# Kernel tuning notes

Measured on AMD Instinct MI355X. Metric: run time of the kernel, lower is better.

Reference implementation:

```python
import jax, jax.numpy as jnp
import numpy as np

D_IN = 1024
D_OUT = 1024
CTX_LEN = 2048
BATCH = 4
SEQ = 2048


def setup_inputs() -> dict:
    key = jax.random.key(0)
    kx, kq, kk, kv = jax.random.split(key, 4)
    x = jax.random.normal(kx, (BATCH, SEQ, D_IN), dtype=jnp.float32)
    s = 1.0 / np.sqrt(D_IN)
    # torch nn.Linear weight is (d_out, d_in); store transposed for x @ W
    W_q = jax.random.uniform(kq, (D_IN, D_OUT), dtype=jnp.float32, minval=-s, maxval=s)
    W_k = jax.random.uniform(kk, (D_IN, D_OUT), dtype=jnp.float32, minval=-s, maxval=s)
    W_v = jax.random.uniform(kv, (D_IN, D_OUT), dtype=jnp.float32, minval=-s, maxval=s)
    return {"x": x, "W_q": W_q, "W_k": W_k, "W_v": W_v}


def reference(x, W_q, W_k, W_v):
    b, n, _ = x.shape
    d_out = W_q.shape[1]
    q = x @ W_q            # [b, n, d_out]
    k = x @ W_k
    v = x @ W_v
    scores = jnp.einsum('bqd,bkd->bqk', q, k)  # [b, n, n]
    causal = jnp.triu(jnp.ones((n, n), dtype=bool), k=1)
    scores = jnp.where(causal, -jnp.inf, scores)
    attn = jax.nn.softmax(scores / jnp.sqrt(jnp.float32(d_out)), axis=-1)
    # dropout p=0.0 -> identity
    return jnp.einsum('bqk,bkd->bqd', attn, v)
```

## Files before the change

### kernel.cpp

```cpp
#include <hip/hip_runtime.h>
#include <hip/hip_bf16.h>

#define BATCH 4
#define SEQ   2048
#define DIN   1024
#define DOUT  1024
#define N3    3072
#define MTOT  (BATCH*SEQ)

typedef __hip_bfloat16 bf16;
typedef __attribute__((ext_vector_type(8))) short bf16x8;
typedef __attribute__((ext_vector_type(4))) float f32x4;

#define MFMA(a,b,c) __builtin_amdgcn_mfma_f32_16x16x32_bf16(a,b,c,0,0,0)

union pack4 { bf16 h[4]; uint2 u2; };
union pack8 { bf16 h[8]; bf16x8 v; };

__device__ __forceinline__ void gl16(const bf16* g, bf16* l)
{
    __builtin_amdgcn_global_load_lds(
        (const __attribute__((address_space(1))) void*)g,
        (__attribute__((address_space(3))) void*)l, 16, 0, 0);
}


__global__ __launch_bounds__(256)
void k_prep(const float* __restrict__ x, const float* __restrict__ Wq,
            const float* __restrict__ Wk, const float* __restrict__ Wv,
            bf16* __restrict__ xb, bf16* __restrict__ Wt,
            float* __restrict__ RS)
{
    __shared__ bf16 t[64][68];
    const int bid = blockIdx.x;
    if (bid < 8192) {
        long i = ((long)bid * 256 + threadIdx.x) * 4;
        float4 v = *(const float4*)(x + i);
        pack4 o;
        o.h[0] = __float2bfloat16(v.x);
        o.h[1] = __float2bfloat16(v.y);
        o.h[2] = __float2bfloat16(v.z);
        o.h[3] = __float2bfloat16(v.w);
        *(uint2*)(xb + i) = o.u2;
        return;
    }
    if (bid >= 8960) {
        int i = (bid - 8960) * 1024 + threadIdx.x * 4;
        *(float4*)(RS + i) = make_float4(0.f, 0.f, 0.f, 0.f);
        return;
    }
    const int idx = bid - 8192;
    const int mat = idx >> 8;
    const int rem = idx & 255;
    const int k0 = (rem >> 4) * 64, n0 = (rem & 15) * 64;
    const float* W = (mat == 0) ? Wq : ((mat == 1) ? Wk : Wv);
#pragma unroll
    for (int p = 0; p < 4; ++p) {
        int kr = p * 16 + (threadIdx.x >> 4);
        int c4 = (threadIdx.x & 15) * 4;
        float4 v = *(const float4*)&W[(long)(k0 + kr) * DOUT + n0 + c4];
        t[c4 + 0][kr] = __float2bfloat16(v.x);
        t[c4 + 1][kr] = __float2bfloat16(v.y);
        t[c4 + 2][kr] = __float2bfloat16(v.z);
        t[c4 + 3][kr] = __float2bfloat16(v.w);
    }
    __syncthreads();
    bf16* O = Wt + (long)mat * DIN * DOUT;
#pragma unroll
    for (int i = 0; i < 2; ++i) {
        int l = threadIdx.x + i * 256;
        int n = l >> 3, c8 = (l & 7) * 8;
        pack8 o;
#pragma unroll
        for (int j = 0; j < 8; ++j) o.h[j] = t[n][c8 + j];
        *(bf16x8*)&O[(long)(n0 + n) * DIN + k0 + c8] = o.v;
    }
}


template<int DIAG>
__device__ __forceinline__ void gemm_core(
    const bf16* __restrict__ Ab, long lda,
    const bf16* __restrict__ Bb, long ldb,
    int nk, bf16* __restrict__ As, bf16* __restrict__ Bs,
    f32x4 acc[4][4])
{
    const int tid  = threadIdx.x;
    const int lane = tid & 63;
    const int wave = tid >> 6;
    const int wm = (wave >> 1) * 64;
    const int wn = (wave & 1) * 64;
    const int r  = lane & 15;
    const int qd = lane >> 4;

    const bool skipWave = DIAG && (wn > wm);
    const bool sameOff  = DIAG && (wn == wm);

    const int row0 = tid >> 3;
    const int c    = (tid & 7) ^ (row0 & 7);
    const long aoff = (long)row0 * lda + c * 8;
    const long boff = (long)row0 * ldb + c * 8;
    const long astep = 32 * lda, bstep = 32 * ldb;
    bf16* dA = &As[tid * 8];
    bf16* dB = &Bs[tid * 8];

    for (int kk = 0; kk < nk; ++kk) {
        const bf16* A = Ab + kk * 64 + aoff;
        const bf16* B = Bb + kk * 64 + boff;
#pragma unroll
        for (int i = 0; i < 4; ++i) {
            gl16(A + i * astep, dA + i * 2048);
            gl16(B + i * bstep, dB + i * 2048);
        }
        __syncthreads();
        if (!skipWave) {
#pragma unroll
            for (int ks = 0; ks < 2; ++ks) {
                const int slot = ((ks * 4 + qd) ^ (r & 7)) * 8;
                bf16x8 af[4], bv[4];
#pragma unroll
                for (int mi = 0; mi < 4; ++mi)
                    af[mi] = *(const bf16x8*)&As[(wm + mi * 16 + r) * 64 + slot];
#pragma unroll
                for (int ni = 0; ni < 4; ++ni)
                    bv[ni] = *(const bf16x8*)&Bs[(wn + ni * 16 + r) * 64 + slot];
#pragma unroll
                for (int mi = 0; mi < 4; ++mi)
#pragma unroll
                    for (int ni = 0; ni < 4; ++ni) {
                        if (sameOff && ni > mi) continue;
                        acc[mi][ni] = MFMA(af[mi], bv[ni], acc[mi][ni]);
                    }
            }
        }
        __syncthreads();
    }
}


__global__ __launch_bounds__(256)
void k_gemm_qkv(const bf16* __restrict__ xb, const bf16* __restrict__ Wt,
                bf16* __restrict__ QK, bf16* __restrict__ Vt)
{
    __shared__ __align__(16) bf16 smem[17408];
    bf16* As = smem;
    bf16* Bs = smem + 8192;
    const int m0 = blockIdx.y * 128, n0 = blockIdx.x * 128;
    f32x4 acc[4][4] = {};
    gemm_core<0>(xb + (long)m0 * DIN, DIN, Wt + (long)n0 * DIN, DIN, DIN / 64, As, Bs, acc);

    const int tid = threadIdx.x;
    const int lane = tid & 63, wave = tid >> 6;
    const int wm = (wave >> 1) * 64, wn = (wave & 1) * 64;
    const int r = lane & 15, qd = lane >> 4;

    if (n0 < 2048) {
#pragma unroll
        for (int mi = 0; mi < 4; ++mi)
#pragma unroll
            for (int ni = 0; ni < 4; ++ni)
#pragma unroll
                for (int j = 0; j < 4; ++j) {
                    int row = m0 + wm + mi * 16 + qd * 4 + j;
                    int col = n0 + wn + ni * 16 + r;
                    QK[(long)row * 2048 + col] = __float2bfloat16(acc[mi][ni][j]);
                }
    } else {
        const int ld = 136;
        bf16* T = smem;
#pragma unroll
        for (int mi = 0; mi < 4; ++mi)
#pragma unroll
            for (int ni = 0; ni < 4; ++ni) {
                pack4 p;
#pragma unroll
                for (int j = 0; j < 4; ++j) p.h[j] = __float2bfloat16(acc[mi][ni][j]);
                int d_l = wn + ni * 16 + r;
                int s_l = wm + mi * 16 + qd * 4;
                *(uint2*)&T[d_l * ld + s_l] = p.u2;
            }
        __syncthreads();
        const int n0v = n0 - 2048;
        const int bb = m0 >> 11;
        const int s0 = m0 & 2047;
        bf16* Ob = Vt + (long)bb * DOUT * SEQ + s0;
#pragma unroll
        for (int p = 0; p < 8; ++p) {
            int l = tid + p * 256;
            int d = l >> 4, s8 = (l & 15) * 8;
            bf16x8 vv = *(const bf16x8*)&T[d * ld + s8];
            *(bf16x8*)&Ob[(long)(n0v + d) * SEQ + s8] = vv;
        }
    }
}


__global__ __launch_bounds__(256, 3)
void k_gemm_scores(const bf16* __restrict__ QK, bf16* __restrict__ P,
                   float* __restrict__ rowSum)
{
    const int bid = blockIdx.x;
    int b, qt, kt;
    if (bid < 480) {
        b = bid & 3;
        int u = bid >> 2;
        qt = 15;
        while (u >= qt) { u -= qt; --qt; }
        kt = u;
    } else {
        int i = bid - 480;
        b = i & 3;
        qt = kt = i >> 2;
    }

    __shared__ __align__(16) bf16 smem[17408];
    bf16* As = smem;
    bf16* Bs = smem + 8192;
    const bf16* A  = QK + (long)b * SEQ * 2048;
    const bf16* Bt = A + 1024;
    f32x4 acc[4][4] = {};
    if (bid < 480)
        gemm_core<0>(A + (long)qt * 128 * 2048, 2048, Bt + (long)kt * 128 * 2048,
                     2048, DIN / 64, As, Bs, acc);
    else
        gemm_core<1>(A + (long)qt * 128 * 2048, 2048, Bt + (long)kt * 128 * 2048,
                     2048, DIN / 64, As, Bs, acc);

    bf16* Pb = P + (long)b * SEQ * SEQ;
    float* RS = rowSum + b * SEQ;
    const int tid = threadIdx.x;
    const int lane = tid & 63, wave = tid >> 6;
    const int wm = (wave >> 1) * 64, wn = (wave & 1) * 64;
    const int r = lane & 15, qd = lane >> 4;

    const int ld = 136;
    bf16* T = smem;

    float rp[4][4];
#pragma unroll
    for (int mi = 0; mi < 4; ++mi)
#pragma unroll
        for (int j = 0; j < 4; ++j) rp[mi][j] = 0.f;

#pragma unroll
    for (int mi = 0; mi < 4; ++mi)
#pragma unroll
        for (int ni = 0; ni < 4; ++ni)
#pragma unroll
            for (int j = 0; j < 4; ++j) {
                int row_l = wm + mi * 16 + qd * 4 + j;
                int col_l = wn + ni * 16 + r;
                int row = qt * 128 + row_l;
                int col = kt * 128 + col_l;
                float e = (col > row) ? 0.f : __expf(acc[mi][ni][j] * 0.03125f);
                rp[mi][j] += e;
                T[row_l * ld + col_l] = __float2bfloat16(e);
            }
#pragma unroll
    for (int d = 1; d < 16; d <<= 1)
#pragma unroll
        for (int mi = 0; mi < 4; ++mi)
#pragma unroll
            for (int j = 0; j < 4; ++j)
                rp[mi][j] += __shfl_xor(rp[mi][j], d, 64);
    if (r == 0) {
#pragma unroll
        for (int mi = 0; mi < 4; ++mi)
#pragma unroll
            for (int j = 0; j < 4; ++j) {
                int row = qt * 128 + wm + mi * 16 + qd * 4 + j;
                atomicAdd(&RS[row], rp[mi][j]);
            }
    }
    __syncthreads();
#pragma unroll
    for (int p = 0; p < 8; ++p) {
        int l = tid + p * 256;
        int row_l = l >> 4, c8 = (l & 15) * 8;
        bf16x8 vv = *(const bf16x8*)&T[row_l * ld + c8];
        *(bf16x8*)&Pb[(long)(qt * 128 + row_l) * SEQ + kt * 128 + c8] = vv;
    }
}


__global__ __launch_bounds__(256, 3)
void k_gemm_pv(const bf16* __restrict__ P, const bf16* __restrict__ Vt,
               const float* __restrict__ rowSum, float* __restrict__ O)
{
    const int bid = blockIdx.x;
    const int h   = bid & 255;
    const int qt  = (bid < 256) ? (15 - (h >> 5)) : (h >> 5);
    const int b   = (h >> 3) & 3;
    const int nt  = h & 7;
    __shared__ __align__(16) bf16 As[128 * 64];
    __shared__ __align__(16) bf16 Bs[128 * 64];
    const bf16* A  = P + (long)b * SEQ * SEQ + (long)qt * 128 * SEQ;
    const bf16* Bt = Vt + (long)b * DOUT * SEQ;
    const int nk = (qt + 1) * 2;
    f32x4 acc[4][4] = {};
    gemm_core<0>(A, SEQ, Bt + (long)nt * 128 * SEQ, SEQ, nk, As, Bs, acc);

    float* Ob = O + (long)b * SEQ * DOUT;
    const float* RS = rowSum + b * SEQ;
    const int lane = threadIdx.x & 63, wave = threadIdx.x >> 6;
    const int wm = (wave >> 1) * 64, wn = (wave & 1) * 64;
    const int r = lane & 15, qd = lane >> 4;
#pragma unroll
    for (int mi = 0; mi < 4; ++mi)
#pragma unroll
        for (int j = 0; j < 4; ++j) {
            int row = qt * 128 + wm + mi * 16 + qd * 4 + j;
            float inv = 1.0f / RS[row];
#pragma unroll
            for (int ni = 0; ni < 4; ++ni) {
                int col = nt * 128 + wn + ni * 16 + r;
                Ob[(long)row * DOUT + col] = acc[mi][ni][j] * inv;
            }
        }
}


extern "C" void kernel_launch(void* const* d_in, const int* in_sizes, int n_in,
                              void* d_out, int out_size, void* d_ws, size_t ws_size,
                              hipStream_t stream)
{
    const float* x  = (const float*)d_in[0];
    const float* Wq = (const float*)d_in[1];
    const float* Wk = (const float*)d_in[2];
    const float* Wv = (const float*)d_in[3];
    float* out = (float*)d_out;

    char* ws = (char*)d_ws;
    bf16*  xb = (bf16*)(ws);
    bf16*  Wt = (bf16*)(ws + 16777216);
    bf16*  QK = (bf16*)(ws + 23068672);
    bf16*  Vt = (bf16*)(ws + 56623104);
    bf16*  P  = (bf16*)(ws + 73400320);
    float* RS = (float*)(ws + 106954752);

    k_prep<<<dim3(8192 + 768 + 8), 256, 0, stream>>>(x, Wq, Wk, Wv, xb, Wt, RS);
    k_gemm_qkv<<<dim3(N3 / 128, MTOT / 128), 256, 0, stream>>>(xb, Wt, QK, Vt);
    k_gemm_scores<<<dim3(544), 256, 0, stream>>>(QK, P, RS);
    k_gemm_pv<<<dim3(512), 256, 0, stream>>>(P, Vt, RS, out);
}
```

Baseline: 211.0 us.

## Fold Wq·Wkᵀ into one matrix so scores use x instead of K

Rewrites the score computation using the identity q·kᵀ = x·(Wq·Wkᵀ)·xᵀ. The prep kernel computes M = Wq·Wkᵀ once in bf16, the projection GEMM produces x·M and V, and the scores GEMM reads x directly in place of K. This removes one third of the projection GEMM work and the K buffer, and stages scores reads through a narrower row stride. The cost is a small extra 1024³ GEMM inside prep, and rounding the folded matrix to bf16 changes numerics.

```diff
diff --git a/kernel.cpp b/kernel.cpp
--- a/kernel.cpp
+++ b/kernel.cpp
@@ -5,7 +5,6 @@
 #define SEQ   2048
 #define DIN   1024
 #define DOUT  1024
-#define N3    3072
 #define MTOT  (BATCH*SEQ)
 
 typedef __hip_bfloat16 bf16;
@@ -28,13 +27,77 @@
 __global__ __launch_bounds__(256)
 void k_prep(const float* __restrict__ x, const float* __restrict__ Wq,
             const float* __restrict__ Wk, const float* __restrict__ Wv,
-            bf16* __restrict__ xb, bf16* __restrict__ Wt,
-            float* __restrict__ RS)
-{
-    __shared__ bf16 t[64][68];
+            bf16* __restrict__ xb, bf16* __restrict__ Wtv,
+            bf16* __restrict__ Mt, float* __restrict__ RS)
+{
+    __shared__ __align__(16) bf16 smem[8192];
     const int bid = blockIdx.x;
-    if (bid < 8192) {
-        long i = ((long)bid * 256 + threadIdx.x) * 4;
+    const int tid = threadIdx.x;
+
+    if (bid < 256) {
+        bf16* As = smem;
+        bf16* Bs = smem + 4096;
+        const int m0 = (bid >> 4) * 64;
+        const int n0 = (bid & 15) * 64;
+        const int lane = tid & 63, wave = tid >> 6;
+        const int wm = (wave >> 1) * 32, wn = (wave & 1) * 32;
+        const int r = lane & 15, qd = lane >> 4;
+        f32x4 acc[2][2] = {};
+        for (int kk = 0; kk < 16; ++kk) {
+#pragma unroll
+            for (int j = 0; j < 2; ++j) {
+                int ch = tid * 2 + j;
+                int row = ch >> 3, cc = ch & 7;
+                int dst = row * 64 + ((cc ^ (row & 7)) * 8);
+                const float* pa = Wk + (long)(m0 + row) * 1024 + kk * 64 + cc * 8;
+                float4 a0 = *(const float4*)pa, a1 = *(const float4*)(pa + 4);
+                pack8 o;
+                o.h[0] = __float2bfloat16(a0.x); o.h[1] = __float2bfloat16(a0.y);
+                o.h[2] = __float2bfloat16(a0.z); o.h[3] = __float2bfloat16(a0.w);
+                o.h[4] = __float2bfloat16(a1.x); o.h[5] = __float2bfloat16(a1.y);
+                o.h[6] = __float2bfloat16(a1.z); o.h[7] = __float2bfloat16(a1.w);
+                *(bf16x8*)&As[dst] = o.v;
+                const float* pb = Wq + (long)(n0 + row) * 1024 + kk * 64 + cc * 8;
+                float4 b0 = *(const float4*)pb, b1 = *(const float4*)(pb + 4);
+                o.h[0] = __float2bfloat16(b0.x); o.h[1] = __float2bfloat16(b0.y);
+                o.h[2] = __float2bfloat16(b0.z); o.h[3] = __float2bfloat16(b0.w);
+                o.h[4] = __float2bfloat16(b1.x); o.h[5] = __float2bfloat16(b1.y);
+                o.h[6] = __float2bfloat16(b1.z); o.h[7] = __float2bfloat16(b1.w);
+                *(bf16x8*)&Bs[dst] = o.v;
+            }
+            __syncthreads();
+#pragma unroll
+            for (int ks = 0; ks < 2; ++ks) {
+                const int slot = ((ks * 4 + qd) ^ (r & 7)) * 8;
+                bf16x8 af[2], bv[2];
+#pragma unroll
+                for (int mi = 0; mi < 2; ++mi)
+                    af[mi] = *(const bf16x8*)&As[(wm + mi * 16 + r) * 64 + slot];
+#pragma unroll
+                for (int ni = 0; ni < 2; ++ni)
+                    bv[ni] = *(const bf16x8*)&Bs[(wn + ni * 16 + r) * 64 + slot];
+#pragma unroll
+                for (int mi = 0; mi < 2; ++mi)
+#pragma unroll
+                    for (int ni = 0; ni < 2; ++ni)
+                        acc[mi][ni] = MFMA(af[mi], bv[ni], acc[mi][ni]);
+            }
+            __syncthreads();
+        }
+#pragma unroll
+        for (int mi = 0; mi < 2; ++mi)
+#pragma unroll
+            for (int ni = 0; ni < 2; ++ni)
+#pragma unroll
+                for (int j = 0; j < 4; ++j) {
+                    int row = m0 + wm + mi * 16 + qd * 4 + j;
+                    int col = n0 + wn + ni * 16 + r;
+                    Mt[(long)row * 1024 + col] = __float2bfloat16(acc[mi][ni][j]);
+                }
+        return;
+    }
+    if (bid < 8448) {
+        long i = ((long)(bid - 256) * 256 + tid) * 4;
         float4 v = *(const float4*)(x + i);
         pack4 o;
         o.h[0] = __float2bfloat16(v.x);
@@ -44,36 +107,33 @@
         *(uint2*)(xb + i) = o.u2;
         return;
     }
-    if (bid >= 8960) {
-        int i = (bid - 8960) * 1024 + threadIdx.x * 4;
+    if (bid >= 8704) {
+        int i = (bid - 8704) * 1024 + tid * 4;
         *(float4*)(RS + i) = make_float4(0.f, 0.f, 0.f, 0.f);
         return;
     }
-    const int idx = bid - 8192;
-    const int mat = idx >> 8;
-    const int rem = idx & 255;
-    const int k0 = (rem >> 4) * 64, n0 = (rem & 15) * 64;
-    const float* W = (mat == 0) ? Wq : ((mat == 1) ? Wk : Wv);
+    const int idx = bid - 8448;
+    const int k0 = (idx >> 4) * 64, n0 = (idx & 15) * 64;
+    bf16* t = smem;
 #pragma unroll
     for (int p = 0; p < 4; ++p) {
-        int kr = p * 16 + (threadIdx.x >> 4);
-        int c4 = (threadIdx.x & 15) * 4;
-        float4 v = *(const float4*)&W[(long)(k0 + kr) * DOUT + n0 + c4];
-        t[c4 + 0][kr] = __float2bfloat16(v.x);
-        t[c4 + 1][kr] = __float2bfloat16(v.y);
-        t[c4 + 2][kr] = __float2bfloat16(v.z);
-        t[c4 + 3][kr] = __float2bfloat16(v.w);
+        int kr = p * 16 + (tid >> 4);
+        int c4 = (tid & 15) * 4;
+        float4 v = *(const float4*)&Wv[(long)(k0 + kr) * DOUT + n0 + c4];
+        t[(c4 + 0) * 68 + kr] = __float2bfloat16(v.x);
+        t[(c4 + 1) * 68 + kr] = __float2bfloat16(v.y);
+        t[(c4 + 2) * 68 + kr] = __float2bfloat16(v.z);
+        t[(c4 + 3) * 68 + kr] = __float2bfloat16(v.w);
     }
     __syncthreads();
-    bf16* O = Wt + (long)mat * DIN * DOUT;
 #pragma unroll
     for (int i = 0; i < 2; ++i) {
-        int l = threadIdx.x + i * 256;
+        int l = tid + i * 256;
         int n = l >> 3, c8 = (l & 7) * 8;
         pack8 o;
 #pragma unroll
-        for (int j = 0; j < 8; ++j) o.h[j] = t[n][c8 + j];
-        *(bf16x8*)&O[(long)(n0 + n) * DIN + k0 + c8] = o.v;
+        for (int j = 0; j < 8; ++j) o.h[j] = t[n * 68 + c8 + j];
+        *(bf16x8*)&Wtv[(long)(n0 + n) * DIN + k0 + c8] = o.v;
     }
 }
 
@@ -139,22 +199,27 @@
 
 
 __global__ __launch_bounds__(256)
-void k_gemm_qkv(const bf16* __restrict__ xb, const bf16* __restrict__ Wt,
-                bf16* __restrict__ QK, bf16* __restrict__ Vt)
+void k_gemm_qkv(const bf16* __restrict__ xb, const bf16* __restrict__ Mt,
+                const bf16* __restrict__ Wtv, bf16* __restrict__ Qp,
+                bf16* __restrict__ Vt)
 {
     __shared__ __align__(16) bf16 smem[17408];
     bf16* As = smem;
     bf16* Bs = smem + 8192;
-    const int m0 = blockIdx.y * 128, n0 = blockIdx.x * 128;
+    const int m0 = blockIdx.y * 128;
+    const int bx = blockIdx.x;
+    const int n0 = bx * 128;
+    const bf16* Bpan = (bx < 8) ? (Mt + (long)n0 * DIN)
+                                : (Wtv + (long)(n0 - 1024) * DIN);
     f32x4 acc[4][4] = {};
-    gemm_core<0>(xb + (long)m0 * DIN, DIN, Wt + (long)n0 * DIN, DIN, DIN / 64, As, Bs, acc);
+    gemm_core<0>(xb + (long)m0 * DIN, DIN, Bpan, DIN, DIN / 64, As, Bs, acc);
 
     const int tid = threadIdx.x;
     const int lane = tid & 63, wave = tid >> 6;
     const int wm = (wave >> 1) * 64, wn = (wave & 1) * 64;
     const int r = lane & 15, qd = lane >> 4;
 
-    if (n0 < 2048) {
+    if (bx < 8) {
 #pragma unroll
         for (int mi = 0; mi < 4; ++mi)
 #pragma unroll
@@ -163,7 +228,7 @@
                 for (int j = 0; j < 4; ++j) {
                     int row = m0 + wm + mi * 16 + qd * 4 + j;
                     int col = n0 + wn + ni * 16 + r;
-                    QK[(long)row * 2048 + col] = __float2bfloat16(acc[mi][ni][j]);
+                    Qp[(long)row * 1024 + col] = __float2bfloat16(acc[mi][ni][j]);
                 }
     } else {
         const int ld = 136;
@@ -180,7 +245,7 @@
                 *(uint2*)&T[d_l * ld + s_l] = p.u2;
             }
         __syncthreads();
-        const int n0v = n0 - 2048;
+        const int n0v = n0 - 1024;
         const int bb = m0 >> 11;
         const int s0 = m0 & 2047;
         bf16* Ob = Vt + (long)bb * DOUT * SEQ + s0;
@@ -196,35 +261,31 @@
 
 
 __global__ __launch_bounds__(256, 3)
-void k_gemm_scores(const bf16* __restrict__ QK, bf16* __restrict__ P,
-                   float* __restrict__ rowSum)
+void k_gemm_scores(const bf16* __restrict__ Qp, const bf16* __restrict__ xb,
+                   bf16* __restrict__ P, float* __restrict__ rowSum)
 {
     const int bid = blockIdx.x;
-    int b, qt, kt;
-    if (bid < 480) {
-        b = bid & 3;
-        int u = bid >> 2;
+    int b, qt, kt, u = -1, d = -1;
+    if      (bid < 256) u = bid;
+    else if (bid < 288) d = bid - 256;
+    else if (bid < 512) u = bid - 32;
+    else                d = bid - 480;
+    if (u >= 0) {
+        b = u & 3;
+        int v = u >> 2;
         qt = 15;
-        while (u >= qt) { u -= qt; --qt; }
-        kt = u;
-    } else {
-        int i = bid - 480;
-        b = i & 3;
-        qt = kt = i >> 2;
-    }
+        while (v >= qt) { v -= qt; --qt; }
+        kt = v;
+    } else { b = d & 3; qt = kt = d >> 2; }
 
     __shared__ __align__(16) bf16 smem[17408];
     bf16* As = smem;
     bf16* Bs = smem + 8192;
-    const bf16* A  = QK + (long)b * SEQ * 2048;
-    const bf16* Bt = A + 1024;
+    const bf16* A  = Qp + (long)(b * SEQ + qt * 128) * 1024;
+    const bf16* Bt = xb + (long)(b * SEQ + kt * 128) * 1024;
     f32x4 acc[4][4] = {};
-    if (bid < 480)
-        gemm_core<0>(A + (long)qt * 128 * 2048, 2048, Bt + (long)kt * 128 * 2048,
-                     2048, DIN / 64, As, Bs, acc);
-    else
-        gemm_core<1>(A + (long)qt * 128 * 2048, 2048, Bt + (long)kt * 128 * 2048,
-                     2048, DIN / 64, As, Bs, acc);
+    if (u >= 0) gemm_core<0>(A, 1024, Bt, 1024, DIN / 64, As, Bs, acc);
+    else        gemm_core<1>(A, 1024, Bt, 1024, DIN / 64, As, Bs, acc);
 
     bf16* Pb = P + (long)b * SEQ * SEQ;
     float* RS = rowSum + b * SEQ;
@@ -257,12 +318,12 @@
                 T[row_l * ld + col_l] = __float2bfloat16(e);
             }
 #pragma unroll
-    for (int d = 1; d < 16; d <<= 1)
+    for (int dd = 1; dd < 16; dd <<= 1)
 #pragma unroll
         for (int mi = 0; mi < 4; ++mi)
 #pragma unroll
             for (int j = 0; j < 4; ++j)
-                rp[mi][j] += __shfl_xor(rp[mi][j], d, 64);
+                rp[mi][j] += __shfl_xor(rp[mi][j], dd, 64);
     if (r == 0) {
 #pragma unroll
         for (int mi = 0; mi < 4; ++mi)
@@ -331,15 +392,17 @@
     float* out = (float*)d_out;
 
     char* ws = (char*)d_ws;
-    bf16*  xb = (bf16*)(ws);
-    bf16*  Wt = (bf16*)(ws + 16777216);
-    bf16*  QK = (bf16*)(ws + 23068672);
-    bf16*  Vt = (bf16*)(ws + 56623104);
-    bf16*  P  = (bf16*)(ws + 73400320);
-    float* RS = (float*)(ws + 106954752);
-
-    k_prep<<<dim3(8192 + 768 + 8), 256, 0, stream>>>(x, Wq, Wk, Wv, xb, Wt, RS);
-    k_gemm_qkv<<<dim3(N3 / 128, MTOT / 128), 256, 0, stream>>>(xb, Wt, QK, Vt);
-    k_gemm_scores<<<dim3(544), 256, 0, stream>>>(QK, P, RS);
+    bf16*  xb  = (bf16*)(ws);
+    bf16*  Wtv = (bf16*)(ws + 16777216);
+    bf16*  Mt  = (bf16*)(ws + 18874368);
+    bf16*  Qp  = (bf16*)(ws + 20971520);
+    bf16*  Vt  = (bf16*)(ws + 37748736);
+    bf16*  P   = (bf16*)(ws + 54525952);
+    float* RS  = (float*)(ws + 88080384);
+
+    k_prep<<<dim3(256 + 8192 + 256 + 8), 256, 0, stream>>>(
+        x, Wq, Wk, Wv, xb, Wtv, Mt, RS);
+    k_gemm_qkv<<<dim3(16, MTOT / 128), 256, 0, stream>>>(xb, Mt, Wtv, Qp, Vt);
+    k_gemm_scores<<<dim3(544), 256, 0, stream>>>(Qp, xb, P, RS);
     k_gemm_pv<<<dim3(512), 256, 0, stream>>>(P, Vt, RS, out);
 }
```

Result: slower. 216.1 us (+2.4%).
